# Kernel tuning notes

Hardware: AMD Instinct MI355X
Metric: run time of the kernel (lower is better)

## Reference

```python
import jax, jax.numpy as jnp
import numpy as np

EMBED_DIM = 256
EPS = 1e-5  # torch F.instance_norm default eps


def setup_inputs() -> dict:
    key = jax.random.key(0)
    ks = jax.random.split(key, 11)
    B, Nq, Nm, C = 4, 4096, 4096, EMBED_DIM
    s = 1.0 / np.sqrt(C)
    return {
        "query": jax.random.normal(ks[0], (B, Nq, C), jnp.float32),
        "key": jax.random.normal(ks[1], (B, Nm, C), jnp.float32),
        "value": jax.random.normal(ks[2], (B, Nm, C), jnp.float32),
        "Wq": jax.random.normal(ks[3], (C, C), jnp.float32) * s,
        "bq": jnp.zeros((C,), jnp.float32),
        "Wk": jax.random.normal(ks[4], (C, C), jnp.float32) * s,
        "bk": jnp.zeros((C,), jnp.float32),
        "Wv": jax.random.normal(ks[5], (C, C), jnp.float32) * s,
        "bv": jnp.zeros((C,), jnp.float32),
        "Wm": jax.random.normal(ks[6], (C, C), jnp.float32) * s,
        "bm": jnp.zeros((C,), jnp.float32),
    }


def reference(query, key, value, Wq, bq, Wk, bk, Wv, bv, Wm, bm):
    # Linear projections (torch nn.Linear: x @ W.T + b)
    q = query @ Wq.T + bq   # [B, Nq, C]
    k = key @ Wk.T + bk     # [B, Nm, C]
    v = value @ Wv.T + bv   # [B, Nm, C]

    attn = jnp.einsum('bnc,bmc->bnm', q, k)  # [B, Nq, Nm]

    # F.instance_norm on [B, Nq, Nm]: N=B, C=Nq, spatial=Nm -> normalize each
    # row over the last dim with biased variance, eps=1e-5, no affine.
    mu = jnp.mean(attn, axis=-1, keepdims=True)
    var = jnp.mean(jnp.square(attn - mu), axis=-1, keepdims=True)
    attn = (attn - mu) * jax.lax.rsqrt(var + EPS)

    # use_softmax=True branch
    attn = attn * (EMBED_DIM ** -0.5)
    attn = jax.nn.softmax(attn, axis=-1)

    out = jnp.einsum('bnm,bmc->bnc', attn, v)  # [B, Nq, C]

    # add_residual=True branch
    return (query + out) @ Wm.T + bm
```

## Files before the change

kernel.cpp:

```cpp
#include <hip/hip_runtime.h>
#include <hip/hip_bf16.h>
#include <cmath>

#define CD 256
#define NQ 4096
#define NM 4096
#define NB 4
#define NTOT (NB*NQ)

typedef __bf16 bf16;
typedef __attribute__((ext_vector_type(8))) __bf16 bf16x8;
typedef __attribute__((ext_vector_type(4))) __bf16 bf16x4;
typedef __attribute__((ext_vector_type(4))) float f32x4;

#define MFMA(a,b,c) __builtin_amdgcn_mfma_f32_16x16x32_bf16(a,b,c,0,0,0)

__global__ __launch_bounds__(256) void cvt_w_kernel(
    const float* __restrict__ wq, const float* __restrict__ wk,
    const float* __restrict__ wv, const float* __restrict__ wm,
    bf16* __restrict__ out)
{
    int i = (blockIdx.x*256 + threadIdx.x)*4;
    const float* srcs[4] = {wq, wk, wv, wm};
    #pragma unroll
    for (int m=0;m<4;++m){
        f32x4 v = *(const f32x4*)(srcs[m]+i);
        bf16x4 o;
        #pragma unroll
        for (int e=0;e<4;++e) o[e] = (bf16)v[e];
        *(bf16x4*)(out + m*65536 + i) = o;
    }
}

template<int MODE>
__global__ __launch_bounds__(256) void proj_kernel(
    const float* __restrict__ X, const bf16* __restrict__ W,
    const float* __restrict__ bias, bf16* __restrict__ out)
{
    const int wave = threadIdx.x>>6, lane = threadIdx.x&63;
    const int lr = lane&15, lg = lane>>4;
    const int n0 = (blockIdx.x>>2)*64 + wave*16;
    const int co0 = (blockIdx.x&3)*64;

    bf16x8 xf[8];
    {
        const float* xr = X + (size_t)(n0+lr)*CD + lg*8;
        #pragma unroll
        for (int ch=0; ch<8; ++ch){
            f32x4 a = *(const f32x4*)(xr + ch*32);
            f32x4 b = *(const f32x4*)(xr + ch*32 + 4);
            bf16x8 t;
            #pragma unroll
            for (int e=0;e<4;++e){ t[e]=(bf16)a[e]; t[4+e]=(bf16)b[e]; }
            xf[ch]=t;
        }
    }
    f32x4 acc[4];
    #pragma unroll
    for (int t=0;t<4;++t) acc[t]=(f32x4){0,0,0,0};

    #pragma unroll
    for (int t=0;t<4;++t){
        const bf16* wr = W + (size_t)(co0+t*16+lr)*CD + lg*8;
        #pragma unroll
        for (int ch=0; ch<8; ++ch){
            bf16x8 wf = *(const bf16x8*)(wr + ch*32);
            if (MODE==0) acc[t] = MFMA(wf, xf[ch], acc[t]);
            else         acc[t] = MFMA(xf[ch], wf, acc[t]);
        }
    }

    if (MODE==0){
        const int n = n0 + lr;
        #pragma unroll
        for (int t=0;t<4;++t){
            int co = co0 + t*16 + 4*lg;
            bf16x4 o;
            #pragma unroll
            for (int r=0;r<4;++r) o[r] = (bf16)(acc[t][r] + bias[co+r]);
            *(bf16x4*)(out + (size_t)n*CD + co) = o;
        }
    } else {
        const int b = n0 / NM;
        const int m0 = (n0 % NM) + 4*lg;
        #pragma unroll
        for (int t=0;t<4;++t){
            int co = co0 + t*16 + lr;
            float bb = bias[co];
            bf16x4 o;
            #pragma unroll
            for (int r=0;r<4;++r) o[r] = (bf16)(acc[t][r] + bb);
            *(bf16x4*)(out + (size_t)b*CD*NM + (size_t)co*NM + m0) = o;
        }
    }
}

__global__ __launch_bounds__(256) void stats_kernel(
    const bf16* __restrict__ q, const bf16* __restrict__ k,
    float* __restrict__ spart)
{
    __shared__ __align__(16) bf16 K_lds[32][264];
    const int wave = threadIdx.x>>6, lane = threadIdx.x&63;
    const int lr = lane&15, lg = lane>>4;
    const int qt = blockIdx.x>>2, slice = blockIdx.x&3;
    const int n0 = qt*64;
    const int b = n0 / NQ;
    const bf16* kb = k + (size_t)b*NM*CD;
    const int row16 = n0 + wave*16;

    bf16x8 qf[8];
    const bf16* qr = q + (size_t)(row16+lr)*CD + lg*8;
    #pragma unroll
    for (int ch=0; ch<8; ++ch) qf[ch] = *(const bf16x8*)(qr + ch*32);

    float sum[4]={0,0,0,0}, ssq[4]={0,0,0,0}, mx[4];
    #pragma unroll
    for (int r=0;r<4;++r) mx[r] = -3.0e38f;

    const int jbeg = slice*(NM/4);
    for (int it=0; it<(NM/4)/32; ++it){
        const int j0 = jbeg + it*32;
        #pragma unroll
        for (int kk=0;kk<4;++kk){
            int id = threadIdx.x + kk*256;
            int r = id>>5, cb = id&31;
            bf16x8 v = *(const bf16x8*)(kb + (size_t)(j0+r)*CD + cb*8);
            *(bf16x8*)&K_lds[r][cb*8] = v;
        }
        __syncthreads();
        f32x4 s0=(f32x4){0,0,0,0}, s1=(f32x4){0,0,0,0};
        #pragma unroll
        for (int ch=0; ch<8; ++ch){
            s0 = MFMA(qf[ch], *(const bf16x8*)&K_lds[lr][lg*8+ch*32], s0);
            s1 = MFMA(qf[ch], *(const bf16x8*)&K_lds[16+lr][lg*8+ch*32], s1);
        }
        __syncthreads();
        #pragma unroll
        for (int r=0;r<4;++r){
            float a = s0[r], c = s1[r];
            sum[r] += a + c;
            ssq[r] = fmaf(a,a,ssq[r]); ssq[r] = fmaf(c,c,ssq[r]);
            mx[r] = fmaxf(mx[r], fmaxf(a, c));
        }
    }
    #pragma unroll
    for (int off=1; off<16; off<<=1){
        #pragma unroll
        for (int r=0;r<4;++r){
            sum[r] += __shfl_xor(sum[r], off);
            ssq[r] += __shfl_xor(ssq[r], off);
            mx[r]  = fmaxf(mx[r], __shfl_xor(mx[r], off));
        }
    }
    if (lr==0){
        #pragma unroll
        for (int r=0;r<4;++r){
            int row = row16 + 4*lg + r;
            size_t idx = ((size_t)row*4 + slice)*3;
            spart[idx+0] = sum[r];
            spart[idx+1] = ssq[r];
            spart[idx+2] = mx[r];
        }
    }
}

__global__ __launch_bounds__(256) void statsfin_kernel(
    const float* __restrict__ spart, float* __restrict__ stats)
{
    int row = blockIdx.x*256 + threadIdx.x;
    float S=0, Q=0, M=-3.0e38f;
    #pragma unroll
    for (int s=0;s<4;++s){
        size_t idx = ((size_t)row*4 + s)*3;
        S += spart[idx+0];
        Q += spart[idx+1];
        M  = fmaxf(M, spart[idx+2]);
    }
    float mean = S * (1.0f/NM);
    float var  = Q * (1.0f/NM) - mean*mean;
    float rstd = rsqrtf(fmaxf(var,0.0f) + 1e-5f);
    stats[row*2+0] = M;
    stats[row*2+1] = rstd * (1.0f/16.0f) * 1.4426950408889634f;
}

__global__ __launch_bounds__(256) void flash_kernel(
    const bf16* __restrict__ q, const bf16* __restrict__ k,
    const bf16* __restrict__ vt, const float* __restrict__ stats,
    bf16* __restrict__ opart, float* __restrict__ dpart)
{
    __shared__ __align__(16) bf16 K_lds[32][264];
    __shared__ __align__(16) bf16 P_lds[64][40];
    const int wave = threadIdx.x>>6, lane = threadIdx.x&63;
    const int lr = lane&15, lg = lane>>4;
    const int qt = blockIdx.x>>2, slice = blockIdx.x&3;
    const int n0 = qt*64;
    const int b = n0 / NQ;
    const bf16* kb = k  + (size_t)b*NM*CD;
    const bf16* vb = vt + (size_t)b*CD*NM + (size_t)(wave*64)*NM;
    const int row16 = n0 + wave*16;

    bf16x8 qf[8];
    const bf16* qr = q + (size_t)(row16+lr)*CD + lg*8;
    #pragma unroll
    for (int ch=0; ch<8; ++ch) qf[ch] = *(const bf16x8*)(qr + ch*32);

    float mxr[4], a2r[4];
    #pragma unroll
    for (int r=0;r<4;++r){
        int row = row16 + 4*lg + r;
        mxr[r] = stats[row*2+0];
        a2r[r] = stats[row*2+1];
    }

    f32x4 oacc[4][4];
    #pragma unroll
    for (int rt=0;rt<4;++rt)
        #pragma unroll
        for (int ct=0;ct<4;++ct) oacc[rt][ct]=(f32x4){0,0,0,0};
    float denom[4]={0,0,0,0};

    const int jbeg = slice*(NM/4);
    for (int it=0; it<(NM/4)/32; ++it){
        const int j0 = jbeg + it*32;
        #pragma unroll
        for (int kk=0;kk<4;++kk){
            int id = threadIdx.x + kk*256;
            int r = id>>5, cb = id&31;
            bf16x8 v = *(const bf16x8*)(kb + (size_t)(j0+r)*CD + cb*8);
            *(bf16x8*)&K_lds[r][cb*8] = v;
        }
        __syncthreads();
        f32x4 s0=(f32x4){0,0,0,0}, s1=(f32x4){0,0,0,0};
        #pragma unroll
        for (int ch=0; ch<8; ++ch){
            s0 = MFMA(qf[ch], *(const bf16x8*)&K_lds[lr][lg*8+ch*32], s0);
            s1 = MFMA(qf[ch], *(const bf16x8*)&K_lds[16+lr][lg*8+ch*32], s1);
        }
        #pragma unroll
        for (int r=0;r<4;++r){
            float p0 = exp2f((s0[r]-mxr[r])*a2r[r]);
            float p1 = exp2f((s1[r]-mxr[r])*a2r[r]);
            denom[r] += p0 + p1;
            P_lds[wave*16+4*lg+r][lr]    = (bf16)p0;
            P_lds[wave*16+4*lg+r][16+lr] = (bf16)p1;
        }
        __syncthreads();
        bf16x8 pf[4];
        #pragma unroll
        for (int rt=0;rt<4;++rt)
            pf[rt] = *(const bf16x8*)&P_lds[rt*16+lr][lg*8];
        #pragma unroll
        for (int ct=0;ct<4;++ct){
            bf16x8 vf = *(const bf16x8*)(vb + (size_t)(ct*16+lr)*NM + j0 + lg*8);
            #pragma unroll
            for (int rt=0;rt<4;++rt)
                oacc[rt][ct] = MFMA(pf[rt], vf, oacc[rt][ct]);
        }
    }

    #pragma unroll
    for (int off=1; off<16; off<<=1){
        #pragma unroll
        for (int r=0;r<4;++r) denom[r] += __shfl_xor(denom[r], off);
    }
    if (lr==0){
        #pragma unroll
        for (int r=0;r<4;++r)
            dpart[(size_t)slice*NTOT + row16 + 4*lg + r] = denom[r];
    }
    #pragma unroll
    for (int rt=0;rt<4;++rt){
        #pragma unroll
        for (int ct=0;ct<4;++ct){
            #pragma unroll
            for (int r=0;r<4;++r){
                int row = n0 + rt*16 + 4*lg + r;
                int co  = wave*64 + ct*16 + lr;
                opart[((size_t)slice*NTOT + row)*CD + co] = (bf16)oacc[rt][ct][r];
            }
        }
    }
}

__global__ __launch_bounds__(256) void combine_kernel(
    const bf16* __restrict__ opart, const float* __restrict__ dpart,
    const float* __restrict__ query, bf16* __restrict__ u)
{
    int gid = blockIdx.x*256 + threadIdx.x;
    int row = gid>>5, c0 = (gid&31)*8;
    float dsum = dpart[row] + dpart[NTOT+row] + dpart[2*NTOT+row] + dpart[3*(size_t)NTOT+row];
    float inv = 1.0f/dsum;
    float acc[8]={0,0,0,0,0,0,0,0};
    #pragma unroll
    for (int s=0;s<4;++s){
        bf16x8 o = *(const bf16x8*)&opart[((size_t)s*NTOT+row)*CD + c0];
        #pragma unroll
        for (int e=0;e<8;++e) acc[e] += (float)o[e];
    }
    f32x4 qa = *(const f32x4*)(query + (size_t)row*CD + c0);
    f32x4 qb = *(const f32x4*)(query + (size_t)row*CD + c0 + 4);
    bf16x8 out;
    #pragma unroll
    for (int e=0;e<4;++e){
        out[e]   = (bf16)(qa[e] + acc[e]*inv);
        out[4+e] = (bf16)(qb[e] + acc[4+e]*inv);
    }
    *(bf16x8*)&u[(size_t)row*CD + c0] = out;
}

__global__ __launch_bounds__(256) void final_kernel(
    const bf16* __restrict__ U, const bf16* __restrict__ W,
    const float* __restrict__ bias, float* __restrict__ out)
{
    const int wave = threadIdx.x>>6, lane = threadIdx.x&63;
    const int lr = lane&15, lg = lane>>4;
    const int n0 = (blockIdx.x>>2)*64 + wave*16;
    const int co0 = (blockIdx.x&3)*64;

    bf16x8 uf[8];
    const bf16* ur = U + (size_t)(n0+lr)*CD + lg*8;
    #pragma unroll
    for (int ch=0; ch<8; ++ch) uf[ch] = *(const bf16x8*)(ur + ch*32);

    f32x4 acc[4];
    #pragma unroll
    for (int t=0;t<4;++t) acc[t]=(f32x4){0,0,0,0};

    #pragma unroll
    for (int t=0;t<4;++t){
        const bf16* wr = W + (size_t)(co0+t*16+lr)*CD + lg*8;
        #pragma unroll
        for (int ch=0; ch<8; ++ch)
            acc[t] = MFMA(*(const bf16x8*)(wr+ch*32), uf[ch], acc[t]);
    }
    const int n = n0 + lr;
    #pragma unroll
    for (int t=0;t<4;++t){
        int co = co0 + t*16 + 4*lg;
        f32x4 o;
        #pragma unroll
        for (int r=0;r<4;++r) o[r] = acc[t][r] + bias[co+r];
        *(f32x4*)(out + (size_t)n*CD + co) = o;
    }
}

extern "C" void kernel_launch(void* const* d_in, const int* in_sizes, int n_in,
                              void* d_out, int out_size, void* d_ws, size_t ws_size,
                              hipStream_t stream)
{
    const float* query = (const float*)d_in[0];
    const float* key_  = (const float*)d_in[1];
    const float* value = (const float*)d_in[2];
    const float* Wq = (const float*)d_in[3];
    const float* bq = (const float*)d_in[4];
    const float* Wk = (const float*)d_in[5];
    const float* bk = (const float*)d_in[6];
    const float* Wv = (const float*)d_in[7];
    const float* bv = (const float*)d_in[8];
    const float* Wm = (const float*)d_in[9];
    const float* bm = (const float*)d_in[10];
    float* out = (float*)d_out;

    bf16* wsb = (bf16*)d_ws;
    bf16* wqb = wsb;
    bf16* wkb = wqb + 65536;
    bf16* wvb = wkb + 65536;
    bf16* wmb = wvb + 65536;
    bf16* qbuf  = wsb + 4*65536;
    bf16* kbuf  = qbuf  + (size_t)NTOT*CD;
    bf16* vtbuf = kbuf  + (size_t)NTOT*CD;
    bf16* ubuf  = vtbuf + (size_t)NTOT*CD;
    float* statsbuf = (float*)(ubuf + (size_t)NTOT*CD);
    float* spart    = statsbuf + (size_t)NTOT*2;
    float* dpart    = spart + (size_t)NTOT*12;
    bf16*  opart    = (bf16*)(dpart + (size_t)NTOT*4);

    cvt_w_kernel<<<64,256,0,stream>>>(Wq, Wk, Wv, Wm, wsb);
    proj_kernel<0><<<1024,256,0,stream>>>(query, wqb, bq, qbuf);
    proj_kernel<0><<<1024,256,0,stream>>>(key_,  wkb, bk, kbuf);
    proj_kernel<1><<<1024,256,0,stream>>>(value, wvb, bv, vtbuf);
    stats_kernel<<<1024,256,0,stream>>>(qbuf, kbuf, spart);
    statsfin_kernel<<<64,256,0,stream>>>(spart, statsbuf);
    flash_kernel<<<1024,256,0,stream>>>(qbuf, kbuf, vtbuf, statsbuf, opart, dpart);
    combine_kernel<<<2048,256,0,stream>>>(opart, dpart, query, ubuf);
    final_kernel<<<1024,256,0,stream>>>(ubuf, wmb, bm, out);
}
```

Before: 382.6 us.

## Compute row stats via K Gram matrix and widen flash kernel to 128 rows

Replaces the full QK^T stats pass with an algebraic form: row means come from q·sum(K) and row sums of squares from q^T (K^T K) q, computed with a per-batch Gram matrix. The softmax shift switches from the row max to the row mean times scale, which assumes normalized scores stay bounded (instance norm makes this roughly safe). The flash kernel now uses 512 threads over 128 query rows, prefetches K tiles into registers, and drops one barrier per iteration. The Gram is rounded to bf16, which may lose variance accuracy, and the mean-based shift risks exp overflow for outlier rows.

```diff
diff --git a/kernel.cpp b/kernel.cpp
--- a/kernel.cpp
+++ b/kernel.cpp
@@ -95,17 +95,155 @@
     }
 }
 
-__global__ __launch_bounds__(256) void stats_kernel(
+__global__ __launch_bounds__(256) void ksum_kernel(
+    const bf16* __restrict__ k, float* __restrict__ kpart)
+{
+    const int b = blockIdx.x>>3, jc = blockIdx.x&7;
+    const int c = threadIdx.x;
+    const bf16* kb = k + (size_t)b*NM*CD + (size_t)(jc*512)*CD;
+    float s = 0.0f;
+    for (int jj=0; jj<512; ++jj) s += (float)kb[(size_t)jj*CD + c];
+    kpart[(b*8+jc)*256 + c] = s;
+}
+
+__global__ __launch_bounds__(256) void gram_kernel(
+    const bf16* __restrict__ k, float* __restrict__ gpart)
+{
+    __shared__ __align__(16) bf16 Kt[256][40];
+    const int wave = threadIdx.x>>6, lane = threadIdx.x&63;
+    const int lr = lane&15, lg = lane>>4;
+    const int b = blockIdx.x>>4, ct = (blockIdx.x>>2)&3, jc = blockIdx.x&3;
+    const bf16* kb = k + (size_t)b*NM*CD;
+
+    f32x4 acc[16];
+    #pragma unroll
+    for (int t=0;t<16;++t) acc[t]=(f32x4){0,0,0,0};
+
+    for (int it=0; it<32; ++it){
+        const int j0 = jc*1024 + it*32;
+        #pragma unroll
+        for (int l=0;l<4;++l){
+            int flat = threadIdx.x + l*256;
+            int jj = flat>>5, cb = flat&31;
+            bf16x8 v = *(const bf16x8*)(kb + (size_t)(j0+jj)*CD + cb*8);
+            #pragma unroll
+            for (int e=0;e<8;++e) Kt[cb*8+e][jj] = v[e];
+        }
+        __syncthreads();
+        bf16x8 af = *(const bf16x8*)&Kt[ct*64 + wave*16 + lr][lg*8];
+        #pragma unroll
+        for (int t=0;t<16;++t){
+            bf16x8 bf = *(const bf16x8*)&Kt[t*16+lr][lg*8];
+            acc[t] = MFMA(af, bf, acc[t]);
+        }
+        __syncthreads();
+    }
+    #pragma unroll
+    for (int t=0;t<16;++t){
+        #pragma unroll
+        for (int r=0;r<4;++r){
+            int c  = ct*64 + wave*16 + 4*lg + r;
+            int cp = t*16 + lr;
+            gpart[(((size_t)jc*4 + b)*256 + c)*256 + cp] = acc[t][r];
+        }
+    }
+}
+
+__global__ __launch_bounds__(256) void gfin_kernel(
+    const float* __restrict__ gpart, bf16* __restrict__ gbf)
+{
+    int gid = blockIdx.x*256 + threadIdx.x;
+    int b = gid>>16, idx = gid&65535;
+    float s = 0.0f;
+    #pragma unroll
+    for (int jc=0;jc<4;++jc) s += gpart[((size_t)jc*4 + b)*65536 + idx];
+    gbf[(size_t)b*65536 + idx] = (bf16)s;
+}
+
+__global__ __launch_bounds__(256) void rowstats_kernel(
+    const bf16* __restrict__ q, const bf16* __restrict__ gbf,
+    const float* __restrict__ kpart, float* __restrict__ stats)
+{
+    __shared__ float ksum[256];
+    const int wave = threadIdx.x>>6, lane = threadIdx.x&63;
+    const int lr = lane&15, lg = lane>>4;
+    const int n0 = blockIdx.x*64;
+    const int b = n0 / NQ;
+    const int row16 = n0 + wave*16;
+    {
+        int c = threadIdx.x;
+        float s = 0.0f;
+        #pragma unroll
+        for (int p=0;p<8;++p) s += kpart[(b*8+p)*256 + c];
+        ksum[c] = s;
+    }
+    __syncthreads();
+
+    bf16x8 qf[8];
+    const bf16* qr = q + (size_t)(row16+lr)*CD + lg*8;
+    #pragma unroll
+    for (int ch=0; ch<8; ++ch) qf[ch] = *(const bf16x8*)(qr + ch*32);
+
+    const bf16* gb = gbf + (size_t)b*65536;
+    f32x4 acc[16];
+    #pragma unroll
+    for (int t=0;t<16;++t) acc[t]=(f32x4){0,0,0,0};
+    #pragma unroll
+    for (int t=0;t<16;++t){
+        #pragma unroll
+        for (int ch=0; ch<8; ++ch){
+            bf16x8 bf = *(const bf16x8*)&gb[(size_t)(t*16+lr)*256 + ch*32 + lg*8];
+            acc[t] = MFMA(qf[ch], bf, acc[t]);
+        }
+    }
+    float msq[4]={0,0,0,0}, mean[4]={0,0,0,0};
+    #pragma unroll
+    for (int t=0;t<16;++t){
+        float ks = ksum[t*16+lr];
+        #pragma unroll
+        for (int r=0;r<4;++r){
+            float qv = (float)q[(size_t)(row16+4*lg+r)*CD + t*16+lr];
+            msq[r]  = fmaf(acc[t][r], qv, msq[r]);
+            mean[r] = fmaf(qv, ks, mean[r]);
+        }
+    }
+    #pragma unroll
+    for (int off=1; off<16; off<<=1){
+        #pragma unroll
+        for (int r=0;r<4;++r){
+            msq[r]  += __shfl_xor(msq[r], off);
+            mean[r] += __shfl_xor(mean[r], off);
+        }
+    }
+    if (lr==0){
+        #pragma unroll
+        for (int r=0;r<4;++r){
+            int row = row16 + 4*lg + r;
+            float mu = mean[r]*(1.0f/NM);
+            float ms = msq[r]*(1.0f/NM);
+            float var = ms - mu*mu;
+            float rstd = rsqrtf(fmaxf(var,0.0f) + 1e-5f);
+            float a2 = rstd * (1.0f/16.0f) * 1.4426950408889634f;
+            stats[row*2+0] = mu*a2;
+            stats[row*2+1] = a2;
+        }
+    }
+}
+
+__global__ __launch_bounds__(512) void flash_kernel(
     const bf16* __restrict__ q, const bf16* __restrict__ k,
-    float* __restrict__ spart)
+    const bf16* __restrict__ vt, const float* __restrict__ stats,
+    bf16* __restrict__ opart, float* __restrict__ dpart)
 {
     __shared__ __align__(16) bf16 K_lds[32][264];
+    __shared__ __align__(16) bf16 P_lds[128][40];
     const int wave = threadIdx.x>>6, lane = threadIdx.x&63;
     const int lr = lane&15, lg = lane>>4;
     const int qt = blockIdx.x>>2, slice = blockIdx.x&3;
-    const int n0 = qt*64;
+    const int n0 = qt*128;
     const int b = n0 / NQ;
-    const bf16* kb = k + (size_t)b*NM*CD;
+    const bf16* kb = k  + (size_t)b*NM*CD;
+    const bf16* vb = vt + (size_t)b*CD*NM + (size_t)(wave*32)*NM;
     const int row16 = n0 + wave*16;
 
     bf16x8 qf[8];
@@ -113,148 +251,61 @@
     #pragma unroll
     for (int ch=0; ch<8; ++ch) qf[ch] = *(const bf16x8*)(qr + ch*32);
 
-    float sum[4]={0,0,0,0}, ssq[4]={0,0,0,0}, mx[4];
-    #pragma unroll
-    for (int r=0;r<4;++r) mx[r] = -3.0e38f;
+    float c2r[4], a2r[4];
+    #pragma unroll
+    for (int r=0;r<4;++r){
+        int row = row16 + 4*lg + r;
+        c2r[r] = stats[row*2+0];
+        a2r[r] = stats[row*2+1];
+    }
+
+    f32x4 oacc[8][2];
+    #pragma unroll
+    for (int rt=0;rt<8;++rt){ oacc[rt][0]=(f32x4){0,0,0,0}; oacc[rt][1]=(f32x4){0,0,0,0}; }
+    float denom[4]={0,0,0,0};
 
     const int jbeg = slice*(NM/4);
-    for (int it=0; it<(NM/4)/32; ++it){
+    bf16x8 kreg0, kreg1;
+    {
+        int f0 = threadIdx.x, f1 = threadIdx.x + 512;
+        kreg0 = *(const bf16x8*)(kb + (size_t)(jbeg + (f0>>5))*CD + (f0&31)*8);
+        kreg1 = *(const bf16x8*)(kb + (size_t)(jbeg + (f1>>5))*CD + (f1&31)*8);
+    }
+    for (int it=0; it<32; ++it){
         const int j0 = jbeg + it*32;
-        #pragma unroll
-        for (int kk=0;kk<4;++kk){
-            int id = threadIdx.x + kk*256;
-            int r = id>>5, cb = id&31;
-            bf16x8 v = *(const bf16x8*)(kb + (size_t)(j0+r)*CD + cb*8);
-            *(bf16x8*)&K_lds[r][cb*8] = v;
+        {
+            int f0 = threadIdx.x, f1 = threadIdx.x + 512;
+            *(bf16x8*)&K_lds[f0>>5][(f0&31)*8] = kreg0;
+            *(bf16x8*)&K_lds[f1>>5][(f1&31)*8] = kreg1;
         }
         __syncthreads();
+        if (it < 31){
+            int f0 = threadIdx.x, f1 = threadIdx.x + 512;
+            kreg0 = *(const bf16x8*)(kb + (size_t)(j0+32 + (f0>>5))*CD + (f0&31)*8);
+            kreg1 = *(const bf16x8*)(kb + (size_t)(j0+32 + (f1>>5))*CD + (f1&31)*8);
+        }
         f32x4 s0=(f32x4){0,0,0,0}, s1=(f32x4){0,0,0,0};
         #pragma unroll
         for (int ch=0; ch<8; ++ch){
             s0 = MFMA(qf[ch], *(const bf16x8*)&K_lds[lr][lg*8+ch*32], s0);
             s1 = MFMA(qf[ch], *(const bf16x8*)&K_lds[16+lr][lg*8+ch*32], s1);
         }
-        __syncthreads();
         #pragma unroll
         for (int r=0;r<4;++r){
-            float a = s0[r], c = s1[r];
-            sum[r] += a + c;
-            ssq[r] = fmaf(a,a,ssq[r]); ssq[r] = fmaf(c,c,ssq[r]);
-            mx[r] = fmaxf(mx[r], fmaxf(a, c));
-        }
-    }
-    #pragma unroll
-    for (int off=1; off<16; off<<=1){
-        #pragma unroll
-        for (int r=0;r<4;++r){
-            sum[r] += __shfl_xor(sum[r], off);
-            ssq[r] += __shfl_xor(ssq[r], off);
-            mx[r]  = fmaxf(mx[r], __shfl_xor(mx[r], off));
-        }
-    }
-    if (lr==0){
-        #pragma unroll
-        for (int r=0;r<4;++r){
-            int row = row16 + 4*lg + r;
-            size_t idx = ((size_t)row*4 + slice)*3;
-            spart[idx+0] = sum[r];
-            spart[idx+1] = ssq[r];
-            spart[idx+2] = mx[r];
-        }
-    }
-}
-
-__global__ __launch_bounds__(256) void statsfin_kernel(
-    const float* __restrict__ spart, float* __restrict__ stats)
-{
-    int row = blockIdx.x*256 + threadIdx.x;
-    float S=0, Q=0, M=-3.0e38f;
-    #pragma unroll
-    for (int s=0;s<4;++s){
-        size_t idx = ((size_t)row*4 + s)*3;
-        S += spart[idx+0];
-        Q += spart[idx+1];
-        M  = fmaxf(M, spart[idx+2]);
-    }
-    float mean = S * (1.0f/NM);
-    float var  = Q * (1.0f/NM) - mean*mean;
-    float rstd = rsqrtf(fmaxf(var,0.0f) + 1e-5f);
-    stats[row*2+0] = M;
-    stats[row*2+1] = rstd * (1.0f/16.0f) * 1.4426950408889634f;
-}
-
-__global__ __launch_bounds__(256) void flash_kernel(
-    const bf16* __restrict__ q, const bf16* __restrict__ k,
-    const bf16* __restrict__ vt, const float* __restrict__ stats,
-    bf16* __restrict__ opart, float* __restrict__ dpart)
-{
-    __shared__ __align__(16) bf16 K_lds[32][264];
-    __shared__ __align__(16) bf16 P_lds[64][40];
-    const int wave = threadIdx.x>>6, lane = threadIdx.x&63;
-    const int lr = lane&15, lg = lane>>4;
-    const int qt = blockIdx.x>>2, slice = blockIdx.x&3;
-    const int n0 = qt*64;
-    const int b = n0 / NQ;
-    const bf16* kb = k  + (size_t)b*NM*CD;
-    const bf16* vb = vt + (size_t)b*CD*NM + (size_t)(wave*64)*NM;
-    const int row16 = n0 + wave*16;
-
-    bf16x8 qf[8];
-    const bf16* qr = q + (size_t)(row16+lr)*CD + lg*8;
-    #pragma unroll
-    for (int ch=0; ch<8; ++ch) qf[ch] = *(const bf16x8*)(qr + ch*32);
-
-    float mxr[4], a2r[4];
-    #pragma unroll
-    for (int r=0;r<4;++r){
-        int row = row16 + 4*lg + r;
-        mxr[r] = stats[row*2+0];
-        a2r[r] = stats[row*2+1];
-    }
-
-    f32x4 oacc[4][4];
-    #pragma unroll
-    for (int rt=0;rt<4;++rt)
-        #pragma unroll
-        for (int ct=0;ct<4;++ct) oacc[rt][ct]=(f32x4){0,0,0,0};
-    float denom[4]={0,0,0,0};
-
-    const int jbeg = slice*(NM/4);
-    for (int it=0; it<(NM/4)/32; ++it){
-        const int j0 = jbeg + it*32;
-        #pragma unroll
-        for (int kk=0;kk<4;++kk){
-            int id = threadIdx.x + kk*256;
-            int r = id>>5, cb = id&31;
-            bf16x8 v = *(const bf16x8*)(kb + (size_t)(j0+r)*CD + cb*8);
-            *(bf16x8*)&K_lds[r][cb*8] = v;
-        }
-        __syncthreads();
-        f32x4 s0=(f32x4){0,0,0,0}, s1=(f32x4){0,0,0,0};
-        #pragma unroll
-        for (int ch=0; ch<8; ++ch){
-            s0 = MFMA(qf[ch], *(const bf16x8*)&K_lds[lr][lg*8+ch*32], s0);
-            s1 = MFMA(qf[ch], *(const bf16x8*)&K_lds[16+lr][lg*8+ch*32], s1);
-        }
-        #pragma unroll
-        for (int r=0;r<4;++r){
-            float p0 = exp2f((s0[r]-mxr[r])*a2r[r]);
-            float p1 = exp2f((s1[r]-mxr[r])*a2r[r]);
+            float p0 = exp2f(s0[r]*a2r[r] - c2r[r]);
+            float p1 = exp2f(s1[r]*a2r[r] - c2r[r]);
             denom[r] += p0 + p1;
             P_lds[wave*16+4*lg+r][lr]    = (bf16)p0;
             P_lds[wave*16+4*lg+r][16+lr] = (bf16)p1;
         }
         __syncthreads();
-        bf16x8 pf[4];
-        #pragma unroll
-        for (int rt=0;rt<4;++rt)
-            pf[rt] = *(const bf16x8*)&P_lds[rt*16+lr][lg*8];
-        #pragma unroll
-        for (int ct=0;ct<4;++ct){
-            bf16x8 vf = *(const bf16x8*)(vb + (size_t)(ct*16+lr)*NM + j0 + lg*8);
-            #pragma unroll
-            for (int rt=0;rt<4;++rt)
-                oacc[rt][ct] = MFMA(pf[rt], vf, oacc[rt][ct]);
+        bf16x8 vf0 = *(const bf16x8*)(vb + (size_t)lr*NM      + j0 + lg*8);
+        bf16x8 vf1 = *(const bf16x8*)(vb + (size_t)(16+lr)*NM + j0 + lg*8);
+        #pragma unroll
+        for (int rt=0;rt<8;++rt){
+            bf16x8 pf = *(const bf16x8*)&P_lds[rt*16+lr][lg*8];
+            oacc[rt][0] = MFMA(pf, vf0, oacc[rt][0]);
+            oacc[rt][1] = MFMA(pf, vf1, oacc[rt][1]);
         }
     }
 
@@ -269,13 +320,13 @@
             dpart[(size_t)slice*NTOT + row16 + 4*lg + r] = denom[r];
     }
     #pragma unroll
-    for (int rt=0;rt<4;++rt){
-        #pragma unroll
-        for (int ct=0;ct<4;++ct){
+    for (int rt=0;rt<8;++rt){
+        #pragma unroll
+        for (int ct=0;ct<2;++ct){
             #pragma unroll
             for (int r=0;r<4;++r){
                 int row = n0 + rt*16 + 4*lg + r;
-                int co  = wave*64 + ct*16 + lr;
+                int co  = wave*32 + ct*16 + lr;
                 opart[((size_t)slice*NTOT + row)*CD + co] = (bf16)oacc[rt][ct][r];
             }
         }
@@ -371,17 +422,21 @@
     bf16* vtbuf = kbuf  + (size_t)NTOT*CD;
     bf16* ubuf  = vtbuf + (size_t)NTOT*CD;
     float* statsbuf = (float*)(ubuf + (size_t)NTOT*CD);
-    float* spart    = statsbuf + (size_t)NTOT*2;
-    float* dpart    = spart + (size_t)NTOT*12;
+    float* kpart    = statsbuf + (size_t)NTOT*2;
+    float* gpart    = kpart + 4*8*256;
+    bf16*  gbf      = (bf16*)(gpart + (size_t)16*65536);
+    float* dpart    = (float*)(gbf + (size_t)4*65536);
     bf16*  opart    = (bf16*)(dpart + (size_t)NTOT*4);
 
     cvt_w_kernel<<<64,256,0,stream>>>(Wq, Wk, Wv, Wm, wsb);
     proj_kernel<0><<<1024,256,0,stream>>>(query, wqb, bq, qbuf);
     proj_kernel<0><<<1024,256,0,stream>>>(key_,  wkb, bk, kbuf);
     proj_kernel<1><<<1024,256,0,stream>>>(value, wvb, bv, vtbuf);
-    stats_kernel<<<1024,256,0,stream>>>(qbuf, kbuf, spart);
-    statsfin_kernel<<<64,256,0,stream>>>(spart, statsbuf);
-    flash_kernel<<<1024,256,0,stream>>>(qbuf, kbuf, vtbuf, statsbuf, opart, dpart);
+    ksum_kernel<<<32,256,0,stream>>>(kbuf, kpart);
+    gram_kernel<<<64,256,0,stream>>>(kbuf, gpart);
+    gfin_kernel<<<1024,256,0,stream>>>(gpart, gbf);
+    rowstats_kernel<<<256,256,0,stream>>>(qbuf, gbf, kpart, statsbuf);
+    flash_kernel<<<512,512,0,stream>>>(qbuf, kbuf, vtbuf, statsbuf, opart, dpart);
     combine_kernel<<<2048,256,0,stream>>>(opart, dpart, query, ubuf);
     final_kernel<<<1024,256,0,stream>>>(ubuf, wmb, bm, out);
 }
```

Result: slower. 497.9 us (+30.1%).
